# Optimization experiments

Hardware: AMD Instinct MI355X
Metric: run time of the kernel (lower is better)

## Reference

```python
import jax, jax.numpy as jnp
import numpy as np

B, S, IN_F, OUT_F, RANK = 4, 4096, 4096, 4096, 64

def soft_threshold24(w):
    # 2:4 soft-threshold pruning: groups of 4 along last dim; keep top-2 |w|,
    # soft-threshold by t = 3rd-largest |w| in each group: sign(w)*relu(|w|-t).
    g = w.reshape(w.shape[0], -1, 4)
    a = jnp.abs(g)
    t = jnp.sort(a, axis=-1)[..., 1:2]  # 3rd largest = 2nd smallest of 4
    s = jnp.sign(g) * jnp.maximum(a - t, 0.0)
    return s.reshape(w.shape)

def fake_fp8_mm(a, b):
    # simulated fp8 GEMM per fake_fp8_mm: fp16 operands, fp32 accumulate/output
    return jnp.matmul(a.astype(jnp.float16), b.astype(jnp.float16),
                      preferred_element_type=jnp.float32)

def setup_inputs():
    key = jax.random.key(0)
    k1, k2, k3 = jax.random.split(key, 3)
    x = jax.random.normal(k1, (B, S, IN_F), jnp.float32)
    std_a = float(np.sqrt(2.0 / (IN_F + RANK)))   # xavier_normal_
    std_b = float(np.sqrt(2.0 / (OUT_F + RANK)))
    weight_A = jax.random.normal(k2, (IN_F, RANK), jnp.float32) * std_a
    weight_B = jax.random.normal(k3, (OUT_F, RANK), jnp.float32) * std_b
    bias = jnp.zeros((OUT_F,), jnp.float32)
    scale_A = jnp.float32(1.0)
    scale_B = jnp.float32(1.0)
    return {"x": x, "weight_A": weight_A, "weight_B": weight_B,
            "bias": bias, "scale_A": scale_A, "scale_B": scale_B}

def reference(x, weight_A, weight_B, bias, scale_A, scale_B):
    wA = soft_threshold24(weight_A) * scale_A      # [IN, R], 2:4 sparse along R
    wB = soft_threshold24(weight_B) * scale_B      # [OUT, R], 2:4 sparse along R
    xf = x.reshape(-1, x.shape[-1])                # [N, IN]
    x_proj = fake_fp8_mm(xf, wA)                   # [N, R]   == FP8SparseOp(x, wA.T, None)
    out = fake_fp8_mm(x_proj, wB.T) + bias         # [N, OUT] == FP8SparseOp(x_proj, wB, bias)
    return out.reshape(*x.shape[:-1], OUT_F)
```

## Files before the change

kernel.cpp:

```cpp
#include <hip/hip_runtime.h>
#include <hip/hip_cooperative_groups.h>

namespace cg = cooperative_groups;

#define IN_FEAT 4096
#define OUT_FEAT 4096
#define RANK 64
#define NROWS 16384
#define TM 32
#define BT 512
#define KC2 256
#define SXS 264
#define CT 256
#define WBS 72
#define XP_STRIDE 72
#define KC 256
#define WA_STRIDE 264

typedef _Float16 half_t;
typedef _Float16 f16x4 __attribute__((ext_vector_type(4)));
typedef _Float16 f16x8 __attribute__((ext_vector_type(8)));
typedef float f32x4 __attribute__((ext_vector_type(4)));

__device__ __forceinline__ f16x4 thr4(float4 v, float s) {
    float a0 = fabsf(v.x), a1 = fabsf(v.y), a2 = fabsf(v.z), a3 = fabsf(v.w);
    float lo1 = fminf(a0, a1), hi1 = fmaxf(a0, a1);
    float lo2 = fminf(a2, a3), hi2 = fmaxf(a2, a3);
    float t = fminf(fmaxf(lo1, lo2), fminf(hi1, hi2));
    f16x4 r;
    r[0] = (half_t)(copysignf(fmaxf(a0 - t, 0.0f), v.x) * s);
    r[1] = (half_t)(copysignf(fmaxf(a1 - t, 0.0f), v.y) * s);
    r[2] = (half_t)(copysignf(fmaxf(a2 - t, 0.0f), v.z) * s);
    r[3] = (half_t)(copysignf(fmaxf(a3 - t, 0.0f), v.w) * s);
    return r;
}

__device__ __forceinline__ f16x4 cvt4(f32x4 v) {
    f16x4 h;
    h[0] = (half_t)v[0]; h[1] = (half_t)v[1];
    h[2] = (half_t)v[2]; h[3] = (half_t)v[3];
    return h;
}

__global__ __launch_bounds__(BT) void coop_kernel(
    const float* __restrict__ x, const float* __restrict__ wA,
    const float* __restrict__ wB, const float* __restrict__ bias,
    const float* __restrict__ scaleA, const float* __restrict__ scaleB,
    float* __restrict__ out, half_t* __restrict__ wAT, half_t* __restrict__ wBh)
{
    __shared__ __align__(16) char pool[2 * CT * WBS * 2];
    __shared__ __align__(16) half_t xp[TM][XP_STRIDE];

    half_t (*xs)[TM][SXS]  = (half_t(*)[TM][SXS])pool;
    half_t (*wbs)[CT][WBS] = (half_t(*)[CT][WBS])pool;

    int tid = threadIdx.x;
    int bid = blockIdx.x;

    {
        int id = bid * BT + tid;
        if (id < 65536) {
            int row = id >> 4;
            int gq  = id & 15;
            float s = scaleB[0];
            f16x4 h = thr4(*(const float4*)(wB + (size_t)row * RANK + gq * 4), s);
            *(f16x4*)(wBh + (size_t)row * RANK + gq * 4) = h;
        } else if (id < 65536 + 8192) {
            int t2 = id - 65536;
            int c4 = t2 & 15;
            int k8 = t2 >> 4;
            float s = scaleA[0];
            f16x8 vc0, vc1, vc2, vc3;
#pragma unroll
            for (int i = 0; i < 8; ++i) {
                float4 v = *(const float4*)(wA + (size_t)(k8 * 8 + i) * RANK + c4 * 4);
                f16x4 h = thr4(v, s);
                vc0[i] = h[0]; vc1[i] = h[1]; vc2[i] = h[2]; vc3[i] = h[3];
            }
            *(f16x8*)(wAT + (size_t)(c4 * 4 + 0) * IN_FEAT + k8 * 8) = vc0;
            *(f16x8*)(wAT + (size_t)(c4 * 4 + 1) * IN_FEAT + k8 * 8) = vc1;
            *(f16x8*)(wAT + (size_t)(c4 * 4 + 2) * IN_FEAT + k8 * 8) = vc2;
            *(f16x8*)(wAT + (size_t)(c4 * 4 + 3) * IN_FEAT + k8 * 8) = vc3;
        }
    }
    cg::this_grid().sync();

    int wave = tid >> 6;
    int lane = tid & 63;
    int l16  = lane & 15;
    int g    = lane >> 4;
    int rowbase = bid * TM;
    int stripe  = wave & 1;
    int quad    = wave >> 1;

    {
        int srow = tid >> 4;
        int sseg = tid & 15;
        const float* srcrow = x + (size_t)(rowbase + srow) * IN_FEAT + sseg * 4;

        {
            const f32x4* p = (const f32x4*)(srcrow);
            f32x4 a0 = p[0], a1 = p[16], a2 = p[32], a3 = p[48];
            half_t* dst = &xs[0][srow][sseg * 4];
            *(f16x4*)(dst +   0) = cvt4(a0);
            *(f16x4*)(dst +  64) = cvt4(a1);
            *(f16x4*)(dst + 128) = cvt4(a2);
            *(f16x4*)(dst + 192) = cvt4(a3);
        }
        __syncthreads();

        f32x4 acc = {0, 0, 0, 0};
        const half_t* wcol = wAT + (size_t)(quad * 16 + l16) * IN_FEAT;
        const half_t* arow = &xs[0][stripe * 16 + l16][0];
        const int xsstep = TM * SXS;
        f32x4 ld0, ld1, ld2, ld3;

        for (int c = 0; c < IN_FEAT / KC2; ++c) {
            if (c + 1 < IN_FEAT / KC2) {
                const f32x4* p = (const f32x4*)(srcrow + (c + 1) * KC2);
                ld0 = p[0]; ld1 = p[16]; ld2 = p[32]; ld3 = p[48];
            }
            f16x8 bfr[8];
#pragma unroll
            for (int j = 0; j < 8; ++j)
                bfr[j] = *(const f16x8*)(wcol + c * KC2 + j * 32 + 8 * g);

            const half_t* ar = arow + (c & 1) * xsstep;
#pragma unroll
            for (int j = 0; j < 8; ++j) {
                f16x8 a = *(const f16x8*)(ar + j * 32 + 8 * g);
                acc = __builtin_amdgcn_mfma_f32_16x16x32_f16(a, bfr[j], acc, 0, 0, 0);
            }
            if (c + 1 < IN_FEAT / KC2) {
                half_t* dst = &xs[(c + 1) & 1][srow][sseg * 4];
                *(f16x4*)(dst +   0) = cvt4(ld0);
                *(f16x4*)(dst +  64) = cvt4(ld1);
                *(f16x4*)(dst + 128) = cvt4(ld2);
                *(f16x4*)(dst + 192) = cvt4(ld3);
            }
            __syncthreads();
        }

#pragma unroll
        for (int r = 0; r < 4; ++r)
            xp[stripe * 16 + 4 * g + r][quad * 16 + l16] = (half_t)acc[r];
    }
    __syncthreads();

    {
        const half_t* xprow = &xp[stripe * 16 + l16][0];
        f16x8 a0 = *(const f16x8*)(xprow + 8 * g);
        f16x8 a1 = *(const f16x8*)(xprow + 32 + 8 * g);

        int sc = tid >> 1;
        int sh = tid & 1;

        {
            const half_t* src = wBh + 0 * (CT * RANK) + (size_t)sc * RANK + sh * 32;
            f16x8 w0 = *(const f16x8*)(src + 0);
            f16x8 w1 = *(const f16x8*)(src + 8);
            f16x8 w2 = *(const f16x8*)(src + 16);
            f16x8 w3 = *(const f16x8*)(src + 24);
            half_t* dst = &wbs[0][sc][sh * 32];
            *(f16x8*)(dst + 0)  = w0;
            *(f16x8*)(dst + 8)  = w1;
            *(f16x8*)(dst + 16) = w2;
            *(f16x8*)(dst + 24) = w3;
        }
        __syncthreads();

        for (int ct = 0; ct < OUT_FEAT / CT; ++ct) {
            f16x8 p0, p1, p2, p3;
            if (ct + 1 < OUT_FEAT / CT) {
                const half_t* src = wBh + (size_t)(ct + 1) * (CT * RANK)
                                  + (size_t)sc * RANK + sh * 32;
                p0 = *(const f16x8*)(src + 0);
                p1 = *(const f16x8*)(src + 8);
                p2 = *(const f16x8*)(src + 16);
                p3 = *(const f16x8*)(src + 24);
            }

            const int buf = ct & 1;
#pragma unroll
            for (int f = 0; f < 4; ++f) {
                int cl = quad * 64 + 16 * f + l16;
                f16x8 b0 = *(const f16x8*)&wbs[buf][cl][8 * g];
                f16x8 b1 = *(const f16x8*)&wbs[buf][cl][32 + 8 * g];
                f32x4 acc2 = {0, 0, 0, 0};
                acc2 = __builtin_amdgcn_mfma_f32_16x16x32_f16(a0, b0, acc2, 0, 0, 0);
                acc2 = __builtin_amdgcn_mfma_f32_16x16x32_f16(a1, b1, acc2, 0, 0, 0);
                int col = ct * CT + cl;
                float bv = bias[col];
#pragma unroll
                for (int r = 0; r < 4; ++r)
                    out[(size_t)(rowbase + stripe * 16 + 4 * g + r) * OUT_FEAT + col] = acc2[r] + bv;
            }

            if (ct + 1 < OUT_FEAT / CT) {
                half_t* dst = &wbs[(ct + 1) & 1][sc][sh * 32];
                *(f16x8*)(dst + 0)  = p0;
                *(f16x8*)(dst + 8)  = p1;
                *(f16x8*)(dst + 16) = p2;
                *(f16x8*)(dst + 24) = p3;
            }
            __syncthreads();
        }
    }
}

__global__ __launch_bounds__(256) void fused_kernel(
    const float* __restrict__ x, const float* __restrict__ wA,
    const float* __restrict__ wB, const float* __restrict__ bias,
    const float* __restrict__ scaleA, const float* __restrict__ scaleB,
    float* __restrict__ out)
{
    __shared__ __align__(16) half_t wAsT[RANK][WA_STRIDE];
    __shared__ float xp_part[2][TM][XP_STRIDE];
    __shared__ __align__(16) half_t xp[TM][XP_STRIDE];

    int tid  = threadIdx.x;
    int wave = tid >> 6;
    int lane = tid & 63;
    int l16  = lane & 15;
    int g    = lane >> 4;
    int rowbase = blockIdx.x * TM;
    int stripe  = wave & 1;
    int ks      = wave >> 1;

    float sA = scaleA[0];
    float sB = scaleB[0];

    const float* xrow = x + (size_t)(rowbase + stripe * 16 + l16) * IN_FEAT;
    f32x4 acc[4] = {f32x4{0,0,0,0}, f32x4{0,0,0,0}, f32x4{0,0,0,0}, f32x4{0,0,0,0}};

    for (int chunk = 0; chunk < IN_FEAT / KC; ++chunk) {
        int k0 = chunk * KC;
#pragma unroll
        for (int pp = 0; pp < 2; ++pp) {
            int p = tid + pp * 256;
            int q = p & 15;
            int r = p >> 4;
            f16x8 vc0, vc1, vc2, vc3;
#pragma unroll
            for (int i = 0; i < 8; ++i) {
                float4 v = *(const float4*)(wA + (size_t)(k0 + 8 * r + i) * RANK + 4 * q);
                f16x4 h = thr4(v, sA);
                vc0[i] = h[0]; vc1[i] = h[1]; vc2[i] = h[2]; vc3[i] = h[3];
            }
            *(f16x8*)&wAsT[4 * q + 0][8 * r] = vc0;
            *(f16x8*)&wAsT[4 * q + 1][8 * r] = vc1;
            *(f16x8*)&wAsT[4 * q + 2][8 * r] = vc2;
            *(f16x8*)&wAsT[4 * q + 3][8 * r] = vc3;
        }
        __syncthreads();

#pragma unroll
        for (int it = 0; it < 4; ++it) {
            int kloc = ks * 128 + it * 32;
            float4 xa = *(const float4*)(xrow + k0 + kloc + 8 * g);
            float4 xb = *(const float4*)(xrow + k0 + kloc + 8 * g + 4);
            f16x8 a;
            a[0] = (half_t)xa.x; a[1] = (half_t)xa.y; a[2] = (half_t)xa.z; a[3] = (half_t)xa.w;
            a[4] = (half_t)xb.x; a[5] = (half_t)xb.y; a[6] = (half_t)xb.z; a[7] = (half_t)xb.w;
#pragma unroll
            for (int f = 0; f < 4; ++f) {
                f16x8 b = *(const f16x8*)&wAsT[16 * f + l16][kloc + 8 * g];
                acc[f] = __builtin_amdgcn_mfma_f32_16x16x32_f16(a, b, acc[f], 0, 0, 0);
            }
        }
        __syncthreads();
    }

#pragma unroll
    for (int f = 0; f < 4; ++f)
#pragma unroll
        for (int r = 0; r < 4; ++r)
            xp_part[ks][stripe * 16 + 4 * g + r][16 * f + l16] = acc[f][r];
    __syncthreads();

#pragma unroll
    for (int i = 0; i < (TM * RANK) / 256; ++i) {
        int e = i * 256 + tid;
        int r = e >> 6, c = e & 63;
        xp[r][c] = (half_t)(xp_part[0][r][c] + xp_part[1][r][c]);
    }
    __syncthreads();

    {
        const half_t* xprow = &xp[stripe * 16 + l16][0];
        f16x8 a0 = *(const f16x8*)(xprow + 8 * g);
        f16x8 a1 = *(const f16x8*)(xprow + 32 + 8 * g);

        int cb0 = ks * (OUT_FEAT / 2);
        for (int cb = cb0; cb < cb0 + OUT_FEAT / 2; cb += 16) {
            int col = cb + l16;
            const float* wp = wB + (size_t)col * RANK;
            float4 w00 = *(const float4*)(wp + 8 * g);
            float4 w01 = *(const float4*)(wp + 8 * g + 4);
            float4 w10 = *(const float4*)(wp + 32 + 8 * g);
            float4 w11 = *(const float4*)(wp + 32 + 8 * g + 4);
            f16x4 b00 = thr4(w00, sB), b01 = thr4(w01, sB);
            f16x4 b10 = thr4(w10, sB), b11 = thr4(w11, sB);
            f16x8 b0, b1;
            b0[0]=b00[0]; b0[1]=b00[1]; b0[2]=b00[2]; b0[3]=b00[3];
            b0[4]=b01[0]; b0[5]=b01[1]; b0[6]=b01[2]; b0[7]=b01[3];
            b1[0]=b10[0]; b1[1]=b10[1]; b1[2]=b10[2]; b1[3]=b10[3];
            b1[4]=b11[0]; b1[5]=b11[1]; b1[6]=b11[2]; b1[7]=b11[3];

            f32x4 acc2 = {0, 0, 0, 0};
            acc2 = __builtin_amdgcn_mfma_f32_16x16x32_f16(a0, b0, acc2, 0, 0, 0);
            acc2 = __builtin_amdgcn_mfma_f32_16x16x32_f16(a1, b1, acc2, 0, 0, 0);
            float bv = bias[col];
#pragma unroll
            for (int r = 0; r < 4; ++r)
                out[(size_t)(rowbase + stripe * 16 + 4 * g + r) * OUT_FEAT + col] = acc2[r] + bv;
        }
    }
}

extern "C" void kernel_launch(void* const* d_in, const int* in_sizes, int n_in,
                              void* d_out, int out_size, void* d_ws, size_t ws_size,
                              hipStream_t stream) {
    const float* x      = (const float*)d_in[0];
    const float* wA     = (const float*)d_in[1];
    const float* wB     = (const float*)d_in[2];
    const float* bias   = (const float*)d_in[3];
    const float* scaleA = (const float*)d_in[4];
    const float* scaleB = (const float*)d_in[5];
    float* out = (float*)d_out;

    const size_t WS_NEED = (size_t)RANK * IN_FEAT * 2
                         + (size_t)OUT_FEAT * RANK * 2;

    bool launched = false;
    if (ws_size >= WS_NEED && d_ws != nullptr) {
        half_t* wAT = (half_t*)d_ws;
        half_t* wBh = wAT + (size_t)RANK * IN_FEAT;
        void* args[] = {(void*)&x, (void*)&wA, (void*)&wB, (void*)&bias,
                        (void*)&scaleA, (void*)&scaleB, (void*)&out,
                        (void*)&wAT, (void*)&wBh};
        hipError_t err = hipLaunchCooperativeKernel((void*)coop_kernel,
                                                    dim3(NROWS / TM), dim3(BT),
                                                    args, 0, stream);
        launched = (err == hipSuccess);
    }
    if (!launched) {
        fused_kernel<<<NROWS / TM, 256, 0, stream>>>(x, wA, wB, bias, scaleA, scaleB, out);
    }
}
```

Before: 212.1 us.

## Split projection and expansion across a grid sync with 256x256 output tiles

The cooperative kernel now runs 256 blocks. Each block computes the rank-64 projection for two 32-row subtiles and writes it to a global workspace. After a grid-wide sync, each block computes 256x256 output tiles from shared-memory copies of the projection, wB and bias. The goal is to reuse the projection and wB tiles across many more MFMAs instead of reloading all of wB for every 32-row block. The cost is an extra global round-trip for the projection, a second grid barrier, and half as many resident blocks during the x-streaming phase, which may hide memory latency less well. Scheduling barriers were also added to order the weight and x prefetch loads.

```diff
diff --git a/kernel.cpp b/kernel.cpp
--- a/kernel.cpp
+++ b/kernel.cpp
@@ -9,13 +9,15 @@
 #define NROWS 16384
 #define TM 32
 #define BT 512
+#define NB 256
 #define KC2 256
 #define SXS 264
-#define CT 256
-#define WBS 72
-#define XP_STRIDE 72
+#define BR 256
+#define BC 256
+#define BS 72
 #define KC 256
 #define WA_STRIDE 264
+#define XP_STRIDE 72
 
 typedef _Float16 half_t;
 typedef _Float16 f16x4 __attribute__((ext_vector_type(4)));
@@ -42,17 +44,15 @@
     return h;
 }
 
-__global__ __launch_bounds__(BT) void coop_kernel(
+__global__ __launch_bounds__(BT) void coop_v3(
     const float* __restrict__ x, const float* __restrict__ wA,
     const float* __restrict__ wB, const float* __restrict__ bias,
     const float* __restrict__ scaleA, const float* __restrict__ scaleB,
-    float* __restrict__ out, half_t* __restrict__ wAT, half_t* __restrict__ wBh)
+    float* __restrict__ out, half_t* __restrict__ wAT, half_t* __restrict__ wBh,
+    half_t* __restrict__ xpw)
 {
-    __shared__ __align__(16) char pool[2 * CT * WBS * 2];
-    __shared__ __align__(16) half_t xp[TM][XP_STRIDE];
-
-    half_t (*xs)[TM][SXS]  = (half_t(*)[TM][SXS])pool;
-    half_t (*wbs)[CT][WBS] = (half_t(*)[CT][WBS])pool;
+    __shared__ __align__(16) char pool[BR * BS * 2 + BC * BS * 2];
+    __shared__ float biasl[BC];
 
     int tid = threadIdx.x;
     int bid = blockIdx.x;
@@ -89,119 +89,139 @@
     int lane = tid & 63;
     int l16  = lane & 15;
     int g    = lane >> 4;
-    int rowbase = bid * TM;
-    int stripe  = wave & 1;
-    int quad    = wave >> 1;
 
     {
+        half_t (*xs)[TM][SXS] = (half_t(*)[TM][SXS])pool;
+        int stripe = wave & 1;
+        int quad   = wave >> 1;
         int srow = tid >> 4;
         int sseg = tid & 15;
-        const float* srcrow = x + (size_t)(rowbase + srow) * IN_FEAT + sseg * 4;
+
+        for (int sub = 0; sub < 2; ++sub) {
+            int rowbase = bid * (2 * TM) + sub * TM;
+            const float* srcrow = x + (size_t)(rowbase + srow) * IN_FEAT + sseg * 4;
+
+            {
+                const f32x4* p = (const f32x4*)(srcrow);
+                f32x4 a0 = p[0], a1 = p[16], a2 = p[32], a3 = p[48];
+                half_t* dst = &xs[0][srow][sseg * 4];
+                *(f16x4*)(dst +   0) = cvt4(a0);
+                *(f16x4*)(dst +  64) = cvt4(a1);
+                *(f16x4*)(dst + 128) = cvt4(a2);
+                *(f16x4*)(dst + 192) = cvt4(a3);
+            }
+            __syncthreads();
+
+            f32x4 acc = {0, 0, 0, 0};
+            const half_t* wcol = wAT + (size_t)(quad * 16 + l16) * IN_FEAT;
+            const half_t* arow = &xs[0][stripe * 16 + l16][0];
+            const int xsstep = TM * SXS;
+            f32x4 ld0, ld1, ld2, ld3;
+
+            for (int c = 0; c < IN_FEAT / KC2; ++c) {
+                f16x8 bfr[8];
+#pragma unroll
+                for (int j = 0; j < 8; ++j)
+                    bfr[j] = *(const f16x8*)(wcol + c * KC2 + j * 32 + 8 * g);
+                __builtin_amdgcn_sched_barrier(0);
+                if (c + 1 < IN_FEAT / KC2) {
+                    const f32x4* p = (const f32x4*)(srcrow + (c + 1) * KC2);
+                    ld0 = p[0]; ld1 = p[16]; ld2 = p[32]; ld3 = p[48];
+                }
+                __builtin_amdgcn_sched_barrier(0);
+
+                const half_t* ar = arow + (c & 1) * xsstep;
+#pragma unroll
+                for (int j = 0; j < 8; ++j) {
+                    f16x8 a = *(const f16x8*)(ar + j * 32 + 8 * g);
+                    acc = __builtin_amdgcn_mfma_f32_16x16x32_f16(a, bfr[j], acc, 0, 0, 0);
+                }
+                if (c + 1 < IN_FEAT / KC2) {
+                    half_t* dst = &xs[(c + 1) & 1][srow][sseg * 4];
+                    *(f16x4*)(dst +   0) = cvt4(ld0);
+                    *(f16x4*)(dst +  64) = cvt4(ld1);
+                    *(f16x4*)(dst + 128) = cvt4(ld2);
+                    *(f16x4*)(dst + 192) = cvt4(ld3);
+                }
+                __syncthreads();
+            }
+
+#pragma unroll
+            for (int r = 0; r < 4; ++r)
+                xpw[(size_t)(rowbase + stripe * 16 + 4 * g + r) * RANK + quad * 16 + l16]
+                    = (half_t)acc[r];
+            __syncthreads();
+        }
+    }
+    cg::this_grid().sync();
+
+    {
+        half_t (*xps)[BS] = (half_t(*)[BS])pool;
+        half_t (*wbs)[BS] = (half_t(*)[BS])(pool + BR * BS * 2);
+
+        int rb = (bid >> 2) * BR;
 
         {
-            const f32x4* p = (const f32x4*)(srcrow);
-            f32x4 a0 = p[0], a1 = p[16], a2 = p[32], a3 = p[48];
-            half_t* dst = &xs[0][srow][sseg * 4];
-            *(f16x4*)(dst +   0) = cvt4(a0);
-            *(f16x4*)(dst +  64) = cvt4(a1);
-            *(f16x4*)(dst + 128) = cvt4(a2);
-            *(f16x4*)(dst + 192) = cvt4(a3);
-        }
-        __syncthreads();
-
-        f32x4 acc = {0, 0, 0, 0};
-        const half_t* wcol = wAT + (size_t)(quad * 16 + l16) * IN_FEAT;
-        const half_t* arow = &xs[0][stripe * 16 + l16][0];
-        const int xsstep = TM * SXS;
-        f32x4 ld0, ld1, ld2, ld3;
-
-        for (int c = 0; c < IN_FEAT / KC2; ++c) {
-            if (c + 1 < IN_FEAT / KC2) {
-                const f32x4* p = (const f32x4*)(srcrow + (c + 1) * KC2);
-                ld0 = p[0]; ld1 = p[16]; ld2 = p[32]; ld3 = p[48];
-            }
-            f16x8 bfr[8];
-#pragma unroll
-            for (int j = 0; j < 8; ++j)
-                bfr[j] = *(const f16x8*)(wcol + c * KC2 + j * 32 + 8 * g);
-
-            const half_t* ar = arow + (c & 1) * xsstep;
-#pragma unroll
-            for (int j = 0; j < 8; ++j) {
-                f16x8 a = *(const f16x8*)(ar + j * 32 + 8 * g);
-                acc = __builtin_amdgcn_mfma_f32_16x16x32_f16(a, bfr[j], acc, 0, 0, 0);
-            }
-            if (c + 1 < IN_FEAT / KC2) {
-                half_t* dst = &xs[(c + 1) & 1][srow][sseg * 4];
-                *(f16x4*)(dst +   0) = cvt4(ld0);
-                *(f16x4*)(dst +  64) = cvt4(ld1);
-                *(f16x4*)(dst + 128) = cvt4(ld2);
-                *(f16x4*)(dst + 192) = cvt4(ld3);
+            int row = tid >> 1, h = tid & 1;
+            const half_t* src = xpw + (size_t)(rb + row) * RANK + h * 32;
+            f16x8 v0 = *(const f16x8*)(src + 0);
+            f16x8 v1 = *(const f16x8*)(src + 8);
+            f16x8 v2 = *(const f16x8*)(src + 16);
+            f16x8 v3 = *(const f16x8*)(src + 24);
+            half_t* dst = &xps[row][h * 32];
+            *(f16x8*)(dst + 0)  = v0;
+            *(f16x8*)(dst + 8)  = v1;
+            *(f16x8*)(dst + 16) = v2;
+            *(f16x8*)(dst + 24) = v3;
+        }
+
+        int wrow = (wave & 1) * 128;
+        int wcol = (wave >> 1) * 64;
+
+        for (int t = 0; t < 4; ++t) {
+            int cb = ((bid & 3) * 4 + t) * BC;
+
+            {
+                int col = tid >> 1, h = tid & 1;
+                const half_t* src = wBh + (size_t)(cb + col) * RANK + h * 32;
+                f16x8 v0 = *(const f16x8*)(src + 0);
+                f16x8 v1 = *(const f16x8*)(src + 8);
+                f16x8 v2 = *(const f16x8*)(src + 16);
+                f16x8 v3 = *(const f16x8*)(src + 24);
+                half_t* dst = &wbs[col][h * 32];
+                *(f16x8*)(dst + 0)  = v0;
+                *(f16x8*)(dst + 8)  = v1;
+                *(f16x8*)(dst + 16) = v2;
+                *(f16x8*)(dst + 24) = v3;
+                if (tid < BC) biasl[tid] = bias[cb + tid];
             }
             __syncthreads();
-        }
-
-#pragma unroll
-        for (int r = 0; r < 4; ++r)
-            xp[stripe * 16 + 4 * g + r][quad * 16 + l16] = (half_t)acc[r];
-    }
-    __syncthreads();
-
-    {
-        const half_t* xprow = &xp[stripe * 16 + l16][0];
-        f16x8 a0 = *(const f16x8*)(xprow + 8 * g);
-        f16x8 a1 = *(const f16x8*)(xprow + 32 + 8 * g);
-
-        int sc = tid >> 1;
-        int sh = tid & 1;
-
-        {
-            const half_t* src = wBh + 0 * (CT * RANK) + (size_t)sc * RANK + sh * 32;
-            f16x8 w0 = *(const f16x8*)(src + 0);
-            f16x8 w1 = *(const f16x8*)(src + 8);
-            f16x8 w2 = *(const f16x8*)(src + 16);
-            f16x8 w3 = *(const f16x8*)(src + 24);
-            half_t* dst = &wbs[0][sc][sh * 32];
-            *(f16x8*)(dst + 0)  = w0;
-            *(f16x8*)(dst + 8)  = w1;
-            *(f16x8*)(dst + 16) = w2;
-            *(f16x8*)(dst + 24) = w3;
-        }
-        __syncthreads();
-
-        for (int ct = 0; ct < OUT_FEAT / CT; ++ct) {
-            f16x8 p0, p1, p2, p3;
-            if (ct + 1 < OUT_FEAT / CT) {
-                const half_t* src = wBh + (size_t)(ct + 1) * (CT * RANK)
-                                  + (size_t)sc * RANK + sh * 32;
-                p0 = *(const f16x8*)(src + 0);
-                p1 = *(const f16x8*)(src + 8);
-                p2 = *(const f16x8*)(src + 16);
-                p3 = *(const f16x8*)(src + 24);
-            }
-
-            const int buf = ct & 1;
-#pragma unroll
-            for (int f = 0; f < 4; ++f) {
-                int cl = quad * 64 + 16 * f + l16;
-                f16x8 b0 = *(const f16x8*)&wbs[buf][cl][8 * g];
-                f16x8 b1 = *(const f16x8*)&wbs[buf][cl][32 + 8 * g];
-                f32x4 acc2 = {0, 0, 0, 0};
-                acc2 = __builtin_amdgcn_mfma_f32_16x16x32_f16(a0, b0, acc2, 0, 0, 0);
-                acc2 = __builtin_amdgcn_mfma_f32_16x16x32_f16(a1, b1, acc2, 0, 0, 0);
-                int col = ct * CT + cl;
-                float bv = bias[col];
-#pragma unroll
-                for (int r = 0; r < 4; ++r)
-                    out[(size_t)(rowbase + stripe * 16 + 4 * g + r) * OUT_FEAT + col] = acc2[r] + bv;
-            }
-
-            if (ct + 1 < OUT_FEAT / CT) {
-                half_t* dst = &wbs[(ct + 1) & 1][sc][sh * 32];
-                *(f16x8*)(dst + 0)  = p0;
-                *(f16x8*)(dst + 8)  = p1;
-                *(f16x8*)(dst + 16) = p2;
-                *(f16x8*)(dst + 24) = p3;
+
+            f16x8 bf0[4], bf1[4];
+            float bv[4];
+#pragma unroll
+            for (int ci = 0; ci < 4; ++ci) {
+                int c16 = wcol + ci * 16 + l16;
+                bf0[ci] = *(const f16x8*)&wbs[c16][8 * g];
+                bf1[ci] = *(const f16x8*)&wbs[c16][32 + 8 * g];
+                bv[ci]  = biasl[c16];
+            }
+
+            for (int rt = 0; rt < 8; ++rt) {
+                const half_t* ar = &xps[wrow + rt * 16 + l16][0];
+                f16x8 a0 = *(const f16x8*)(ar + 8 * g);
+                f16x8 a1 = *(const f16x8*)(ar + 32 + 8 * g);
+                int row0 = rb + wrow + rt * 16 + 4 * g;
+#pragma unroll
+                for (int ci = 0; ci < 4; ++ci) {
+                    f32x4 acc2 = {0, 0, 0, 0};
+                    acc2 = __builtin_amdgcn_mfma_f32_16x16x32_f16(a0, bf0[ci], acc2, 0, 0, 0);
+                    acc2 = __builtin_amdgcn_mfma_f32_16x16x32_f16(a1, bf1[ci], acc2, 0, 0, 0);
+                    int col = cb + wcol + ci * 16 + l16;
+#pragma unroll
+                    for (int r = 0; r < 4; ++r)
+                        out[(size_t)(row0 + r) * OUT_FEAT + col] = acc2[r] + bv[ci];
+                }
             }
             __syncthreads();
         }
@@ -329,18 +349,20 @@
     const float* scaleB = (const float*)d_in[5];
     float* out = (float*)d_out;
 
-    const size_t WS_NEED = (size_t)RANK * IN_FEAT * 2
-                         + (size_t)OUT_FEAT * RANK * 2;
+    const size_t WS_V3 = (size_t)RANK * IN_FEAT * 2
+                       + (size_t)OUT_FEAT * RANK * 2
+                       + (size_t)NROWS * RANK * 2;
 
     bool launched = false;
-    if (ws_size >= WS_NEED && d_ws != nullptr) {
+    if (ws_size >= WS_V3 && d_ws != nullptr) {
         half_t* wAT = (half_t*)d_ws;
         half_t* wBh = wAT + (size_t)RANK * IN_FEAT;
+        half_t* xpw = wBh + (size_t)OUT_FEAT * RANK;
         void* args[] = {(void*)&x, (void*)&wA, (void*)&wB, (void*)&bias,
                         (void*)&scaleA, (void*)&scaleB, (void*)&out,
-                        (void*)&wAT, (void*)&wBh};
-        hipError_t err = hipLaunchCooperativeKernel((void*)coop_kernel,
-                                                    dim3(NROWS / TM), dim3(BT),
+                        (void*)&wAT, (void*)&wBh, (void*)&xpw};
+        hipError_t err = hipLaunchCooperativeKernel((void*)coop_v3,
+                                                    dim3(NB), dim3(BT),
                                                     args, 0, stream);
         launched = (err == hipSuccess);
     }
```

Measured after the change: 221.2 us. +4.3%, slower.

## Warp-specialize coop kernel: producer waves compute x_proj while consumers emit output

Applied to the files above, without the earlier changes.

The cooperative kernel now launches 256 blocks of 64 rows each, processed as four 16-row sub-tiles. Four producer waves compute the first GEMM for sub-tile s while four consumer waves compute the second GEMM for sub-tile s-1, reading wB straight from global instead of staging it in shared memory. The intent is to overlap the x-streaming projection with the output-writing GEMM and cut barrier overhead using a custom LDS-only barrier macro. Risks: half the waves per phase may sit idle, and there is an extra pipeline drain step per block.

```diff
diff --git a/kernel.cpp b/kernel.cpp
--- a/kernel.cpp
+++ b/kernel.cpp
@@ -7,20 +7,29 @@
 #define OUT_FEAT 4096
 #define RANK 64
 #define NROWS 16384
+#define BT 512
+#define NB 256
+#define NSUB 4
+#define SROWS 16
+#define KCC 256
+#define XSS 264
+#define XPS 72
 #define TM 32
-#define BT 512
-#define KC2 256
-#define SXS 264
-#define CT 256
-#define WBS 72
-#define XP_STRIDE 72
 #define KC 256
 #define WA_STRIDE 264
+#define XP_STRIDE 72
 
 typedef _Float16 half_t;
 typedef _Float16 f16x4 __attribute__((ext_vector_type(4)));
 typedef _Float16 f16x8 __attribute__((ext_vector_type(8)));
 typedef float f32x4 __attribute__((ext_vector_type(4)));
+
+#define SYNCL() do {                                         \
+    __builtin_amdgcn_sched_barrier(0);                       \
+    asm volatile("s_waitcnt lgkmcnt(0)" ::: "memory");       \
+    __builtin_amdgcn_s_barrier();                            \
+    __builtin_amdgcn_sched_barrier(0);                       \
+} while (0)
 
 __device__ __forceinline__ f16x4 thr4(float4 v, float s) {
     float a0 = fabsf(v.x), a1 = fabsf(v.y), a2 = fabsf(v.z), a3 = fabsf(v.w);
@@ -42,17 +51,14 @@
     return h;
 }
 
-__global__ __launch_bounds__(BT) void coop_kernel(
+__global__ __launch_bounds__(BT) void coop_v4(
     const float* __restrict__ x, const float* __restrict__ wA,
     const float* __restrict__ wB, const float* __restrict__ bias,
     const float* __restrict__ scaleA, const float* __restrict__ scaleB,
     float* __restrict__ out, half_t* __restrict__ wAT, half_t* __restrict__ wBh)
 {
-    __shared__ __align__(16) char pool[2 * CT * WBS * 2];
-    __shared__ __align__(16) half_t xp[TM][XP_STRIDE];
-
-    half_t (*xs)[TM][SXS]  = (half_t(*)[TM][SXS])pool;
-    half_t (*wbs)[CT][WBS] = (half_t(*)[CT][WBS])pool;
+    __shared__ __align__(16) half_t xs[2][SROWS][XSS];
+    __shared__ __align__(16) half_t xpl[2][SROWS][XPS];
 
     int tid = threadIdx.x;
     int bid = blockIdx.x;
@@ -89,121 +95,91 @@
     int lane = tid & 63;
     int l16  = lane & 15;
     int g    = lane >> 4;
-    int rowbase = bid * TM;
-    int stripe  = wave & 1;
-    int quad    = wave >> 1;
-
-    {
-        int srow = tid >> 4;
-        int sseg = tid & 15;
-        const float* srcrow = x + (size_t)(rowbase + srow) * IN_FEAT + sseg * 4;
-
-        {
+    bool prod = wave < 4;
+    int rw   = wave & 3;
+    int rowbase = bid * (NSUB * SROWS);
+
+    int srow = (tid >> 4) & 15;
+    int sseg = tid & 15;
+    const half_t* wcol = wAT + (size_t)(rw * 16 + l16) * IN_FEAT;
+    int cbase = rw * 1024;
+
+    for (int s = 0; s <= NSUB; ++s) {
+        bool pa = prod && (s < NSUB);
+        bool ca = (!prod) && (s > 0);
+
+        int prow0 = rowbase + s * SROWS;
+        int crow0 = rowbase + (s - 1) * SROWS;
+        const float* srcrow = x + (size_t)(prow0 + srow) * IN_FEAT + sseg * 4;
+
+        f32x4 acc = {0, 0, 0, 0};
+        f16x8 a0, a1;
+
+        if (pa) {
             const f32x4* p = (const f32x4*)(srcrow);
-            f32x4 a0 = p[0], a1 = p[16], a2 = p[32], a3 = p[48];
+            f32x4 t0 = p[0], t1 = p[16], t2 = p[32], t3 = p[48];
             half_t* dst = &xs[0][srow][sseg * 4];
-            *(f16x4*)(dst +   0) = cvt4(a0);
-            *(f16x4*)(dst +  64) = cvt4(a1);
-            *(f16x4*)(dst + 128) = cvt4(a2);
-            *(f16x4*)(dst + 192) = cvt4(a3);
-        }
-        __syncthreads();
-
-        f32x4 acc = {0, 0, 0, 0};
-        const half_t* wcol = wAT + (size_t)(quad * 16 + l16) * IN_FEAT;
-        const half_t* arow = &xs[0][stripe * 16 + l16][0];
-        const int xsstep = TM * SXS;
-        f32x4 ld0, ld1, ld2, ld3;
-
-        for (int c = 0; c < IN_FEAT / KC2; ++c) {
-            if (c + 1 < IN_FEAT / KC2) {
-                const f32x4* p = (const f32x4*)(srcrow + (c + 1) * KC2);
-                ld0 = p[0]; ld1 = p[16]; ld2 = p[32]; ld3 = p[48];
-            }
-            f16x8 bfr[8];
-#pragma unroll
-            for (int j = 0; j < 8; ++j)
-                bfr[j] = *(const f16x8*)(wcol + c * KC2 + j * 32 + 8 * g);
-
-            const half_t* ar = arow + (c & 1) * xsstep;
-#pragma unroll
-            for (int j = 0; j < 8; ++j) {
-                f16x8 a = *(const f16x8*)(ar + j * 32 + 8 * g);
-                acc = __builtin_amdgcn_mfma_f32_16x16x32_f16(a, bfr[j], acc, 0, 0, 0);
-            }
-            if (c + 1 < IN_FEAT / KC2) {
-                half_t* dst = &xs[(c + 1) & 1][srow][sseg * 4];
-                *(f16x4*)(dst +   0) = cvt4(ld0);
-                *(f16x4*)(dst +  64) = cvt4(ld1);
-                *(f16x4*)(dst + 128) = cvt4(ld2);
-                *(f16x4*)(dst + 192) = cvt4(ld3);
-            }
-            __syncthreads();
-        }
-
-#pragma unroll
-        for (int r = 0; r < 4; ++r)
-            xp[stripe * 16 + 4 * g + r][quad * 16 + l16] = (half_t)acc[r];
-    }
-    __syncthreads();
-
-    {
-        const half_t* xprow = &xp[stripe * 16 + l16][0];
-        f16x8 a0 = *(const f16x8*)(xprow + 8 * g);
-        f16x8 a1 = *(const f16x8*)(xprow + 32 + 8 * g);
-
-        int sc = tid >> 1;
-        int sh = tid & 1;
-
-        {
-            const half_t* src = wBh + 0 * (CT * RANK) + (size_t)sc * RANK + sh * 32;
-            f16x8 w0 = *(const f16x8*)(src + 0);
-            f16x8 w1 = *(const f16x8*)(src + 8);
-            f16x8 w2 = *(const f16x8*)(src + 16);
-            f16x8 w3 = *(const f16x8*)(src + 24);
-            half_t* dst = &wbs[0][sc][sh * 32];
-            *(f16x8*)(dst + 0)  = w0;
-            *(f16x8*)(dst + 8)  = w1;
-            *(f16x8*)(dst + 16) = w2;
-            *(f16x8*)(dst + 24) = w3;
-        }
-        __syncthreads();
-
-        for (int ct = 0; ct < OUT_FEAT / CT; ++ct) {
-            f16x8 p0, p1, p2, p3;
-            if (ct + 1 < OUT_FEAT / CT) {
-                const half_t* src = wBh + (size_t)(ct + 1) * (CT * RANK)
-                                  + (size_t)sc * RANK + sh * 32;
-                p0 = *(const f16x8*)(src + 0);
-                p1 = *(const f16x8*)(src + 8);
-                p2 = *(const f16x8*)(src + 16);
-                p3 = *(const f16x8*)(src + 24);
-            }
-
-            const int buf = ct & 1;
-#pragma unroll
-            for (int f = 0; f < 4; ++f) {
-                int cl = quad * 64 + 16 * f + l16;
-                f16x8 b0 = *(const f16x8*)&wbs[buf][cl][8 * g];
-                f16x8 b1 = *(const f16x8*)&wbs[buf][cl][32 + 8 * g];
-                f32x4 acc2 = {0, 0, 0, 0};
-                acc2 = __builtin_amdgcn_mfma_f32_16x16x32_f16(a0, b0, acc2, 0, 0, 0);
-                acc2 = __builtin_amdgcn_mfma_f32_16x16x32_f16(a1, b1, acc2, 0, 0, 0);
-                int col = ct * CT + cl;
-                float bv = bias[col];
-#pragma unroll
-                for (int r = 0; r < 4; ++r)
-                    out[(size_t)(rowbase + stripe * 16 + 4 * g + r) * OUT_FEAT + col] = acc2[r] + bv;
-            }
-
-            if (ct + 1 < OUT_FEAT / CT) {
-                half_t* dst = &wbs[(ct + 1) & 1][sc][sh * 32];
-                *(f16x8*)(dst + 0)  = p0;
-                *(f16x8*)(dst + 8)  = p1;
-                *(f16x8*)(dst + 16) = p2;
-                *(f16x8*)(dst + 24) = p3;
-            }
-            __syncthreads();
+            *(f16x4*)(dst +   0) = cvt4(t0);
+            *(f16x4*)(dst +  64) = cvt4(t1);
+            *(f16x4*)(dst + 128) = cvt4(t2);
+            *(f16x4*)(dst + 192) = cvt4(t3);
+        }
+        if (ca) {
+            const half_t* xr = &xpl[(s - 1) & 1][l16][0];
+            a0 = *(const f16x8*)(xr + 8 * g);
+            a1 = *(const f16x8*)(xr + 32 + 8 * g);
+        }
+        SYNCL();
+
+        for (int w = 1; w <= 16; ++w) {
+            if (pa) {
+                int c = w - 1;
+                f16x8 bfr[8];
+#pragma unroll
+                for (int j = 0; j < 8; ++j)
+                    bfr[j] = *(const f16x8*)(wcol + c * KCC + j * 32 + 8 * g);
+                __builtin_amdgcn_sched_barrier(0);
+                f32x4 ld0, ld1, ld2, ld3;
+                if (c + 1 < 16) {
+                    const f32x4* p = (const f32x4*)(srcrow + (c + 1) * KCC);
+                    ld0 = p[0]; ld1 = p[16]; ld2 = p[32]; ld3 = p[48];
+                }
+                __builtin_amdgcn_sched_barrier(0);
+                const half_t* ar = &xs[c & 1][l16][0];
+#pragma unroll
+                for (int j = 0; j < 8; ++j) {
+                    f16x8 a = *(const f16x8*)(ar + j * 32 + 8 * g);
+                    acc = __builtin_amdgcn_mfma_f32_16x16x32_f16(a, bfr[j], acc, 0, 0, 0);
+                }
+                if (c + 1 < 16) {
+                    half_t* dst = &xs[(c + 1) & 1][srow][sseg * 4];
+                    *(f16x4*)(dst +   0) = cvt4(ld0);
+                    *(f16x4*)(dst +  64) = cvt4(ld1);
+                    *(f16x4*)(dst + 128) = cvt4(ld2);
+                    *(f16x4*)(dst + 192) = cvt4(ld3);
+                }
+                if (w == 16) {
+#pragma unroll
+                    for (int r = 0; r < 4; ++r)
+                        xpl[s & 1][4 * g + r][rw * 16 + l16] = (half_t)acc[r];
+                }
+            }
+            if (ca) {
+#pragma unroll
+                for (int q = 0; q < 4; ++q) {
+                    int colf = cbase + ((w - 1) * 4 + q) * 16;
+                    const half_t* wp = wBh + (size_t)(colf + l16) * RANK;
+                    f16x8 wf0 = *(const f16x8*)(wp + 8 * g);
+                    f16x8 wf1 = *(const f16x8*)(wp + 32 + 8 * g);
+                    f32x4 c0 = {0, 0, 0, 0};
+                    c0 = __builtin_amdgcn_mfma_f32_16x16x32_f16(wf0, a0, c0, 0, 0, 0);
+                    c0 = __builtin_amdgcn_mfma_f32_16x16x32_f16(wf1, a1, c0, 0, 0, 0);
+                    f32x4 bv = *(const f32x4*)(bias + colf + 4 * g);
+                    c0[0] += bv[0]; c0[1] += bv[1]; c0[2] += bv[2]; c0[3] += bv[3];
+                    *(f32x4*)&out[(size_t)(crow0 + l16) * OUT_FEAT + colf + 4 * g] = c0;
+                }
+            }
+            SYNCL();
         }
     }
 }
@@ -329,18 +305,18 @@
     const float* scaleB = (const float*)d_in[5];
     float* out = (float*)d_out;
 
-    const size_t WS_NEED = (size_t)RANK * IN_FEAT * 2
-                         + (size_t)OUT_FEAT * RANK * 2;
+    const size_t WS_V4 = (size_t)RANK * IN_FEAT * 2
+                       + (size_t)OUT_FEAT * RANK * 2;
 
     bool launched = false;
-    if (ws_size >= WS_NEED && d_ws != nullptr) {
+    if (ws_size >= WS_V4 && d_ws != nullptr) {
         half_t* wAT = (half_t*)d_ws;
         half_t* wBh = wAT + (size_t)RANK * IN_FEAT;
         void* args[] = {(void*)&x, (void*)&wA, (void*)&wB, (void*)&bias,
                         (void*)&scaleA, (void*)&scaleB, (void*)&out,
                         (void*)&wAT, (void*)&wBh};
-        hipError_t err = hipLaunchCooperativeKernel((void*)coop_kernel,
-                                                    dim3(NROWS / TM), dim3(BT),
+        hipError_t err = hipLaunchCooperativeKernel((void*)coop_v4,
+                                                    dim3(NB), dim3(BT),
                                                     args, 0, stream);
         launched = (err == hipSuccess);
     }
```

New measurement: 250.4 us. 18.0% more time.
